# Optimization experiments

Measured on AMD Instinct MI355X. Metric: run time of the kernel, lower is better.

Reference implementation:

```python
import jax, jax.numpy as jnp
import numpy as np

B, C, CI, H, W = 8, 256, 128, 48, 48


def conv1x1(x, w, b):
    # x: (B,C,H,W), w: (CI,C), b: (CI,)
    return jnp.einsum('bchw,oc->bohw', x, w) + b[None, :, None, None]


def setup_inputs() -> dict:
    key = jax.random.key(0)
    ks = jax.random.split(key, 14)
    s = 1.0 / np.sqrt(C)
    d = {
        'x_1': jax.random.normal(ks[0], (B, C, H, W), jnp.float32),
        'x_2': jax.random.normal(ks[1], (B, C, H, W), jnp.float32),
    }
    names = ['v1', 'k1', 'q1', 'v2', 'k2', 'q2']
    for i, n in enumerate(names):
        d['w_' + n] = jax.random.uniform(ks[2 + 2 * i], (CI, C), jnp.float32, -s, s)
        d['b_' + n] = jax.random.uniform(ks[3 + 2 * i], (CI,), jnp.float32, -s, s)
    return d


def reference(x_1, x_2, w_v1, b_v1, w_k1, b_k1, w_q1, b_q1,
              w_v2, b_v2, w_k2, b_k2, w_q2, b_q2):
    b, ci, h, w = x_1.shape[0], w_v1.shape[0], x_1.shape[2], x_1.shape[3]
    n = h * w
    V1 = conv1x1(x_1, w_v1, b_v1).reshape(b, ci, n)
    K1 = conv1x1(x_1, w_k1, b_k1).reshape(b, ci, n)
    Q1 = conv1x1(x_1, w_q1, b_q1).reshape(b, ci, n)
    V2 = conv1x1(x_2, w_v2, b_v2).reshape(b, ci, n)
    K2 = conv1x1(x_2, w_k2, b_k2).reshape(b, ci, n)
    Q2 = conv1x1(x_2, w_q2, b_q2).reshape(b, ci, n)
    # sigmoid-gated cross attention, (B, N, N)
    R12 = jax.nn.sigmoid(jnp.einsum('bcn,bcm->bnm', Q1, K2))
    R21 = jax.nn.sigmoid(jnp.einsum('bcn,bcm->bnm', Q2, K1))
    Fu1 = jnp.einsum('bnm,bcm->bcn', R12, V2).reshape(b, ci, h, w)
    Fu2 = jnp.einsum('bnm,bcm->bcn', R21, V1).reshape(b, ci, h, w)
    y_1 = jnp.concatenate([x_1, Fu1], axis=1)
    y_2 = jnp.concatenate([x_2, Fu2], axis=1)
    return (y_1, y_2)
```

## Files before the change

### kernel.cpp

```cpp
#include <hip/hip_runtime.h>
#include <hip/hip_bf16.h>


typedef __bf16 bf16;
typedef __bf16 bf16x8 __attribute__((ext_vector_type(8)));
typedef __bf16 bf16x4 __attribute__((ext_vector_type(4)));
typedef float f32x4 __attribute__((ext_vector_type(4)));
typedef float f32x16 __attribute__((ext_vector_type(16)));
typedef unsigned int u32x4 __attribute__((ext_vector_type(4)));

#define NB 8
#define NC 256
#define NCI 128
#define NHW 2304
#define NT32 72

__global__ __launch_bounds__(256) void wconv_kernel(
    const float* __restrict__ w0, const float* __restrict__ w1,
    const float* __restrict__ w2, const float* __restrict__ w3,
    const float* __restrict__ w4, const float* __restrict__ w5,
    bf16* __restrict__ dst)
{
    int idx = (blockIdx.x * 256 + threadIdx.x) * 8;
    int m = idx >> 15;
    int off = idx & 32767;
    const float* w = (m == 0) ? w0 : (m == 1) ? w1 : (m == 2) ? w2
                   : (m == 3) ? w3 : (m == 4) ? w4 : w5;
    f32x4 a0 = *(const f32x4*)(w + off);
    f32x4 a1 = *(const f32x4*)(w + off + 4);
    bf16x8 o;
    #pragma unroll
    for (int j = 0; j < 4; ++j) { o[j] = (bf16)a0[j]; o[4 + j] = (bf16)a1[j]; }
    *(bf16x8*)(dst + idx) = o;
}

__global__ __launch_bounds__(256) void qkv_kernel(
    const float* __restrict__ x1, const float* __restrict__ x2,
    const bf16* __restrict__ wb,
    const float* __restrict__ bv1, const float* __restrict__ bk1, const float* __restrict__ bq1,
    const float* __restrict__ bv2, const float* __restrict__ bk2, const float* __restrict__ bq2,
    bf16* __restrict__ Qt, bf16* __restrict__ Kt, bf16* __restrict__ Vt,
    float* __restrict__ out)
{
    __shared__ __align__(16) bf16 Xt[32 * 264];

    int gid = blockIdx.x;
    int nt = gid % NT32;
    int s = (gid / NT32) & 1;
    int b = gid / (2 * NT32);
    int n0 = nt * 32;

    const float* x = s ? x2 : x1;
    const bf16* wv = wb + (size_t)(s * 3 + 0) * (NCI * NC);
    const bf16* wk = wb + (size_t)(s * 3 + 1) * (NCI * NC);
    const bf16* wq = wb + (size_t)(s * 3 + 2) * (NCI * NC);
    const float* bv = s ? bv2 : bv1;
    const float* bk = s ? bk2 : bk1;
    const float* bq = s ? bq2 : bq1;
    float* outy = out + (size_t)s * (NB * 384 * NHW);

    int tid = threadIdx.x;
    {
        int n_off = (tid & 3) * 8;
        int c0l = tid >> 2;
        #pragma unroll
        for (int i = 0; i < 4; ++i) {
            int c = c0l + i * 64;
            const float* src = x + ((size_t)(b * NC + c) * NHW + n0 + n_off);
            f32x4 a0 = *(const f32x4*)src;
            f32x4 a1 = *(const f32x4*)(src + 4);
            float* dsty = outy + ((size_t)(b * 384 + c) * NHW + n0 + n_off);
            *(f32x4*)dsty = a0;
            *(f32x4*)(dsty + 4) = a1;
            #pragma unroll
            for (int j = 0; j < 4; ++j) {
                Xt[(n_off + j) * 264 + c] = (bf16)a0[j];
                Xt[(n_off + 4 + j) * 264 + c] = (bf16)a1[j];
            }
        }
    }
    __syncthreads();

    int lane = tid & 63;
    int wid = tid >> 6;
    int row = lane & 15, quad = lane >> 4;
    int ci_base = wid * 32;

    f32x4 acc[3][2][2];
    #pragma unroll
    for (int t = 0; t < 3; ++t)
        #pragma unroll
        for (int mi = 0; mi < 2; ++mi)
            #pragma unroll
            for (int j = 0; j < 2; ++j)
                acc[t][mi][j] = (f32x4){0.f, 0.f, 0.f, 0.f};

    const bf16* wptr[3] = {wq, wk, wv};
    #pragma unroll
    for (int ks = 0; ks < 8; ++ks) {
        int c0 = ks * 32 + quad * 8;
        bf16x8 bfrag[2];
        #pragma unroll
        for (int j = 0; j < 2; ++j)
            bfrag[j] = *(const bf16x8*)&Xt[(j * 16 + row) * 264 + c0];
        #pragma unroll
        for (int t = 0; t < 3; ++t) {
            #pragma unroll
            for (int mi = 0; mi < 2; ++mi) {
                bf16x8 afrag = *(const bf16x8*)&wptr[t][(size_t)(ci_base + mi * 16 + row) * NC + c0];
                #pragma unroll
                for (int j = 0; j < 2; ++j)
                    acc[t][mi][j] = __builtin_amdgcn_mfma_f32_16x16x32_bf16(
                        afrag, bfrag[j], acc[t][mi][j], 0, 0, 0);
            }
        }
    }

    size_t qkbase = ((size_t)s * NB + b) * NHW * NCI;
    size_t vbase  = ((size_t)s * NB + b) * NCI * NHW;
    #pragma unroll
    for (int mi = 0; mi < 2; ++mi) {
        int ci0 = ci_base + mi * 16 + quad * 4;
        f32x4 bq4 = *(const f32x4*)&bq[ci0];
        f32x4 bk4 = *(const f32x4*)&bk[ci0];
        f32x4 bv4 = *(const f32x4*)&bv[ci0];
        #pragma unroll
        for (int j = 0; j < 2; ++j) {
            int n = n0 + j * 16 + row;
            bf16x4 pk;
            #pragma unroll
            for (int r = 0; r < 4; ++r) pk[r] = (bf16)(acc[0][mi][j][r] + bq4[r]);
            *(bf16x4*)&Qt[qkbase + (size_t)n * NCI + ci0] = pk;
            #pragma unroll
            for (int r = 0; r < 4; ++r) pk[r] = (bf16)(acc[1][mi][j][r] + bk4[r]);
            *(bf16x4*)&Kt[qkbase + (size_t)n * NCI + ci0] = pk;
            #pragma unroll
            for (int r = 0; r < 4; ++r)
                Vt[vbase + (size_t)(nt * 128 + ci0 + r) * 32 + (j * 16 + row)] =
                    (bf16)(acc[2][mi][j][r] + bv4[r]);
        }
    }
}

__global__ __launch_bounds__(256, 2) void attn_kernel(
    const bf16* __restrict__ Qt, const bf16* __restrict__ Kt, const bf16* __restrict__ Vt,
    float* __restrict__ out)
{
    __shared__ __align__(16) float RED[8192];

    int gid = blockIdx.x;
    int b = gid & 7;
    int dir = (gid >> 3) & 1;
    int nt = gid >> 4;

    int tid = threadIdx.x;
    int lane = tid & 63;
    int mq = tid >> 6;
    int col = lane & 31, hi = lane >> 5;

    int sq = dir, skv = dir ^ 1;
    const bf16* q = Qt + ((size_t)sq  * NB + b) * (NHW * NCI);
    const bf16* k = Kt + ((size_t)skv * NB + b) * (NHW * NCI);
    const bf16* v = Vt + ((size_t)skv * NB + b) * (NCI * NHW);
    float* outy = out + (size_t)dir * (NB * 384 * NHW) + ((size_t)b * 384 + 256) * NHW;

    int nw = nt * 32;

    bf16x8 qf[8];
    #pragma unroll
    for (int j = 0; j < 8; ++j)
        qf[j] = *(const bf16x8*)&q[(size_t)(nw + col) * NCI + j * 16 + hi * 8];

    f32x16 o0, o1, o2, o3;
    #pragma unroll
    for (int j = 0; j < 16; ++j) { o0[j] = 0.f; o1[j] = 0.f; o2[j] = 0.f; o3[j] = 0.f; }

    const bf16* kbase = k + (size_t)(mq * 576 + col) * NCI + hi * 8;
    const bf16* vbase = v + ((size_t)(mq * 18) * 128 + col) * 32 + hi * 8;

    bf16x8 kfA[8], kfB[8];
    #pragma unroll
    for (int j = 0; j < 8; ++j) kfA[j] = *(const bf16x8*)(kbase + j * 16);

    auto body = [&](bf16x8 (&cur)[8], bf16x8 (&nxt)[8], int i) {
        const bf16* vp = vbase + (size_t)i * 4096;
        bf16x8 vf[8];
        #pragma unroll
        for (int ct = 0; ct < 4; ++ct) {
            vf[2 * ct]     = *(const bf16x8*)(vp + ct * 1024);
            vf[2 * ct + 1] = *(const bf16x8*)(vp + ct * 1024 + 16);
        }
        int inx = (i + 1 < 18) ? (i + 1) : 0;
        const bf16* kpn = kbase + (size_t)inx * 32 * NCI;
        #pragma unroll
        for (int j = 0; j < 8; ++j) nxt[j] = *(const bf16x8*)(kpn + j * 16);

        f32x16 s;
        #pragma unroll
        for (int j = 0; j < 16; ++j) s[j] = 0.f;
        __builtin_amdgcn_s_setprio(1);
        #pragma unroll
        for (int j = 0; j < 8; ++j)
            s = __builtin_amdgcn_mfma_f32_32x32x16_bf16(cur[j], qf[j], s, 0, 0, 0);
        __builtin_amdgcn_s_setprio(0);

        #pragma unroll
        for (int r = 0; r < 16; ++r) {
            float e = __expf(-s[r]);
            s[r] = __builtin_amdgcn_rcpf(1.0f + e);
        }
        u32x4 pbw0, pbw1;
        {
            unsigned int a0, a1, c0, c1;
            asm("v_cvt_pk_bf16_f32 %0, %1, %2" : "=v"(a0) : "v"(s[0]), "v"(s[1]));
            asm("v_cvt_pk_bf16_f32 %0, %1, %2" : "=v"(a1) : "v"(s[2]), "v"(s[3]));
            asm("v_cvt_pk_bf16_f32 %0, %1, %2" : "=v"(c0) : "v"(s[4]), "v"(s[5]));
            asm("v_cvt_pk_bf16_f32 %0, %1, %2" : "=v"(c1) : "v"(s[6]), "v"(s[7]));
            asm volatile("v_permlane32_swap_b32 %0, %1" : "+v"(a0), "+v"(c0));
            asm volatile("v_permlane32_swap_b32 %0, %1" : "+v"(a1), "+v"(c1));
            pbw0 = (u32x4){a0, a1, c0, c1};
        }
        {
            unsigned int a0, a1, c0, c1;
            asm("v_cvt_pk_bf16_f32 %0, %1, %2" : "=v"(a0) : "v"(s[8]),  "v"(s[9]));
            asm("v_cvt_pk_bf16_f32 %0, %1, %2" : "=v"(a1) : "v"(s[10]), "v"(s[11]));
            asm("v_cvt_pk_bf16_f32 %0, %1, %2" : "=v"(c0) : "v"(s[12]), "v"(s[13]));
            asm("v_cvt_pk_bf16_f32 %0, %1, %2" : "=v"(c1) : "v"(s[14]), "v"(s[15]));
            asm volatile("v_permlane32_swap_b32 %0, %1" : "+v"(a0), "+v"(c0));
            asm volatile("v_permlane32_swap_b32 %0, %1" : "+v"(a1), "+v"(c1));
            pbw1 = (u32x4){a0, a1, c0, c1};
        }

        __builtin_amdgcn_s_setprio(1);
        {
            bf16x8 pf = __builtin_bit_cast(bf16x8, pbw0);
            o0 = __builtin_amdgcn_mfma_f32_32x32x16_bf16(vf[0], pf, o0, 0, 0, 0);
            o1 = __builtin_amdgcn_mfma_f32_32x32x16_bf16(vf[2], pf, o1, 0, 0, 0);
            o2 = __builtin_amdgcn_mfma_f32_32x32x16_bf16(vf[4], pf, o2, 0, 0, 0);
            o3 = __builtin_amdgcn_mfma_f32_32x32x16_bf16(vf[6], pf, o3, 0, 0, 0);
        }
        {
            bf16x8 pf = __builtin_bit_cast(bf16x8, pbw1);
            o0 = __builtin_amdgcn_mfma_f32_32x32x16_bf16(vf[1], pf, o0, 0, 0, 0);
            o1 = __builtin_amdgcn_mfma_f32_32x32x16_bf16(vf[3], pf, o1, 0, 0, 0);
            o2 = __builtin_amdgcn_mfma_f32_32x32x16_bf16(vf[5], pf, o2, 0, 0, 0);
            o3 = __builtin_amdgcn_mfma_f32_32x32x16_bf16(vf[7], pf, o3, 0, 0, 0);
        }
        __builtin_amdgcn_s_setprio(0);
    };

    #pragma unroll 1
    for (int ii = 0; ii < 9; ++ii) {
        body(kfA, kfB, 2 * ii);
        body(kfB, kfA, 2 * ii + 1);
    }

    float* buf0 = RED;
    float* buf1 = RED + 4096;

    auto wpart = [&](float* buf, const f32x16& a, int cb) {
        #pragma unroll
        for (int g = 0; g < 4; ++g) {
            f32x4 v4;
            #pragma unroll
            for (int j = 0; j < 4; ++j) v4[j] = a[g * 4 + j];
            *(f32x4*)&buf[lane * 64 + (((cb * 4 + g) ^ (lane & 15)) * 4)] = v4;
        }
    };
    auto rpart = [&](float* buf, f32x16& a, int cb) {
        #pragma unroll
        for (int g = 0; g < 4; ++g) {
            f32x4 v4 = *(const f32x4*)&buf[lane * 64 + (((cb * 4 + g) ^ (lane & 15)) * 4)];
            #pragma unroll
            for (int j = 0; j < 4; ++j) a[g * 4 + j] += v4[j];
        }
    };

    __syncthreads();
    if (mq == 2) { wpart(buf0, o0, 0); wpart(buf0, o1, 1); wpart(buf0, o2, 2); wpart(buf0, o3, 3); }
    if (mq == 3) { wpart(buf1, o0, 0); wpart(buf1, o1, 1); wpart(buf1, o2, 2); wpart(buf1, o3, 3); }
    __syncthreads();
    if (mq == 0) { rpart(buf0, o0, 0); rpart(buf0, o1, 1); rpart(buf0, o2, 2); rpart(buf0, o3, 3); }
    if (mq == 1) { rpart(buf1, o0, 0); rpart(buf1, o1, 1); rpart(buf1, o2, 2); rpart(buf1, o3, 3); }
    __syncthreads();
    if (mq == 1) { wpart(buf0, o0, 0); wpart(buf0, o1, 1); wpart(buf0, o2, 2); wpart(buf0, o3, 3); }
    __syncthreads();
    if (mq == 0) {
        rpart(buf0, o0, 0); rpart(buf0, o1, 1); rpart(buf0, o2, 2); rpart(buf0, o3, 3);
        #pragma unroll
        for (int r = 0; r < 16; ++r) {
            int cr = (r & 3) + 8 * (r >> 2) + 4 * hi;
            outy[(size_t)(0 * 32 + cr) * NHW + nw + col] = o0[r];
            outy[(size_t)(1 * 32 + cr) * NHW + nw + col] = o1[r];
            outy[(size_t)(2 * 32 + cr) * NHW + nw + col] = o2[r];
            outy[(size_t)(3 * 32 + cr) * NHW + nw + col] = o3[r];
        }
    }
}

extern "C" void kernel_launch(void* const* d_in, const int* in_sizes, int n_in,
                              void* d_out, int out_size, void* d_ws, size_t ws_size,
                              hipStream_t stream) {
    const float* x1  = (const float*)d_in[0];
    const float* x2  = (const float*)d_in[1];
    const float* wv1 = (const float*)d_in[2];  const float* bv1 = (const float*)d_in[3];
    const float* wk1 = (const float*)d_in[4];  const float* bk1 = (const float*)d_in[5];
    const float* wq1 = (const float*)d_in[6];  const float* bq1 = (const float*)d_in[7];
    const float* wv2 = (const float*)d_in[8];  const float* bv2 = (const float*)d_in[9];
    const float* wk2 = (const float*)d_in[10]; const float* bk2 = (const float*)d_in[11];
    const float* wq2 = (const float*)d_in[12]; const float* bq2 = (const float*)d_in[13];
    float* out = (float*)d_out;

    size_t per = (size_t)2 * NB * NHW * NCI;
    bf16* Qt = (bf16*)d_ws;
    bf16* Kt = Qt + per;
    bf16* Vt = Kt + per;
    bf16* wb = Vt + per;

    wconv_kernel<<<dim3(96), dim3(256), 0, stream>>>(wv1, wk1, wq1, wv2, wk2, wq2, wb);

    qkv_kernel<<<dim3(NB * 2 * NT32), dim3(256), 0, stream>>>(
        x1, x2, wb, bv1, bk1, bq1, bv2, bk2, bq2, Qt, Kt, Vt, out);

    attn_kernel<<<dim3(NB * 2 * NT32), dim3(256), 0, stream>>>(Qt, Kt, Vt, out);
}
```

Before: 284.5 us.

## Split attention block into two query tiles and two key halves

Each attention block now covers 64 query positions, with two waves per 32-query tile. Each of those waves walks half of the key/value sequence (36 steps), where before four waves each took a quarter. This halves the grid, cuts the cross-wave reduction from a 4-way tree to a single 2-way exchange, and lets the two waves sharing a key half read the same K/V data. In exchange, each wave runs a longer serial loop and there are fewer blocks to fill the GPU.

```diff
diff --git a/kernel.cpp b/kernel.cpp
--- a/kernel.cpp
+++ b/kernel.cpp
@@ -155,7 +155,9 @@
 
     int tid = threadIdx.x;
     int lane = tid & 63;
-    int mq = tid >> 6;
+    int w = tid >> 6;
+    int ns = w & 1;
+    int mh = w >> 1;
     int col = lane & 31, hi = lane >> 5;
 
     int sq = dir, skv = dir ^ 1;
@@ -164,7 +166,7 @@
     const bf16* v = Vt + ((size_t)skv * NB + b) * (NCI * NHW);
     float* outy = out + (size_t)dir * (NB * 384 * NHW) + ((size_t)b * 384 + 256) * NHW;
 
-    int nw = nt * 32;
+    int nw = nt * 64 + ns * 32;
 
     bf16x8 qf[8];
     #pragma unroll
@@ -175,8 +177,8 @@
     #pragma unroll
     for (int j = 0; j < 16; ++j) { o0[j] = 0.f; o1[j] = 0.f; o2[j] = 0.f; o3[j] = 0.f; }
 
-    const bf16* kbase = k + (size_t)(mq * 576 + col) * NCI + hi * 8;
-    const bf16* vbase = v + ((size_t)(mq * 18) * 128 + col) * 32 + hi * 8;
+    const bf16* kbase = k + (size_t)(mh * 1152 + col) * NCI + hi * 8;
+    const bf16* vbase = v + ((size_t)(mh * 36) * 128 + col) * 32 + hi * 8;
 
     bf16x8 kfA[8], kfB[8];
     #pragma unroll
@@ -190,7 +192,7 @@
             vf[2 * ct]     = *(const bf16x8*)(vp + ct * 1024);
             vf[2 * ct + 1] = *(const bf16x8*)(vp + ct * 1024 + 16);
         }
-        int inx = (i + 1 < 18) ? (i + 1) : 0;
+        int inx = (i + 1 < 36) ? (i + 1) : 0;
         const bf16* kpn = kbase + (size_t)inx * 32 * NCI;
         #pragma unroll
         for (int j = 0; j < 8; ++j) nxt[j] = *(const bf16x8*)(kpn + j * 16);
@@ -250,43 +252,36 @@
     };
 
     #pragma unroll 1
-    for (int ii = 0; ii < 9; ++ii) {
+    for (int ii = 0; ii < 18; ++ii) {
         body(kfA, kfB, 2 * ii);
         body(kfB, kfA, 2 * ii + 1);
     }
 
-    float* buf0 = RED;
-    float* buf1 = RED + 4096;
-
-    auto wpart = [&](float* buf, const f32x16& a, int cb) {
+    float* buf = RED + ns * 4096;
+
+    auto wpart = [&](float* bp, const f32x16& a, int cb) {
         #pragma unroll
         for (int g = 0; g < 4; ++g) {
             f32x4 v4;
             #pragma unroll
             for (int j = 0; j < 4; ++j) v4[j] = a[g * 4 + j];
-            *(f32x4*)&buf[lane * 64 + (((cb * 4 + g) ^ (lane & 15)) * 4)] = v4;
+            *(f32x4*)&bp[lane * 64 + (((cb * 4 + g) ^ (lane & 15)) * 4)] = v4;
         }
     };
-    auto rpart = [&](float* buf, f32x16& a, int cb) {
+    auto rpart = [&](float* bp, f32x16& a, int cb) {
         #pragma unroll
         for (int g = 0; g < 4; ++g) {
-            f32x4 v4 = *(const f32x4*)&buf[lane * 64 + (((cb * 4 + g) ^ (lane & 15)) * 4)];
+            f32x4 v4 = *(const f32x4*)&bp[lane * 64 + (((cb * 4 + g) ^ (lane & 15)) * 4)];
             #pragma unroll
             for (int j = 0; j < 4; ++j) a[g * 4 + j] += v4[j];
         }
     };
 
     __syncthreads();
-    if (mq == 2) { wpart(buf0, o0, 0); wpart(buf0, o1, 1); wpart(buf0, o2, 2); wpart(buf0, o3, 3); }
-    if (mq == 3) { wpart(buf1, o0, 0); wpart(buf1, o1, 1); wpart(buf1, o2, 2); wpart(buf1, o3, 3); }
+    if (mh == 1) { wpart(buf, o0, 0); wpart(buf, o1, 1); wpart(buf, o2, 2); wpart(buf, o3, 3); }
     __syncthreads();
-    if (mq == 0) { rpart(buf0, o0, 0); rpart(buf0, o1, 1); rpart(buf0, o2, 2); rpart(buf0, o3, 3); }
-    if (mq == 1) { rpart(buf1, o0, 0); rpart(buf1, o1, 1); rpart(buf1, o2, 2); rpart(buf1, o3, 3); }
-    __syncthreads();
-    if (mq == 1) { wpart(buf0, o0, 0); wpart(buf0, o1, 1); wpart(buf0, o2, 2); wpart(buf0, o3, 3); }
-    __syncthreads();
-    if (mq == 0) {
-        rpart(buf0, o0, 0); rpart(buf0, o1, 1); rpart(buf0, o2, 2); rpart(buf0, o3, 3);
+    if (mh == 0) {
+        rpart(buf, o0, 0); rpart(buf, o1, 1); rpart(buf, o2, 2); rpart(buf, o3, 3);
         #pragma unroll
         for (int r = 0; r < 16; ++r) {
             int cr = (r & 3) + 8 * (r >> 2) + 4 * hi;
@@ -322,5 +317,5 @@
     qkv_kernel<<<dim3(NB * 2 * NT32), dim3(256), 0, stream>>>(
         x1, x2, wb, bv1, bk1, bq1, bv2, bk2, bq2, Qt, Kt, Vt, out);
 
-    attn_kernel<<<dim3(NB * 2 * NT32), dim3(256), 0, stream>>>(Qt, Kt, Vt, out);
+    attn_kernel<<<dim3(NB * 2 * 36), dim3(256), 0, stream>>>(Qt, Kt, Vt, out);
 }
```

New measurement: 305.2 us. 7.3% more time.
